# Kernel tuning notes

Hardware: AMD Instinct MI355X
Metric: run time of the kernel (lower is better)

## Reference

```python
import jax, jax.numpy as jnp
import numpy as np

E, H, D, F = 768, 12, 64, 3072
SCALE = D ** -0.5
EPS = 1e-5


def setup_inputs() -> dict:
    key = jax.random.key(0)
    ks = jax.random.split(key, 12)
    B, S = 8, 1024
    x = jax.random.normal(ks[0], (B, S, E), jnp.float32)
    # causal additive mask: 0 on/below diagonal, large negative above
    causal = jnp.triu(jnp.full((S, S), -1e9, jnp.float32), k=1)
    mask = jnp.broadcast_to(causal, (B, 1, S, S))
    init = lambda k, shp: jax.random.normal(k, shp, jnp.float32) * (shp[0] ** -0.5)
    return {
        "x": x, "mask": mask,
        "ln1_g": jnp.ones((E,), jnp.float32), "ln1_b": jnp.zeros((E,), jnp.float32),
        "wq": init(ks[1], (E, E)), "bq": jnp.zeros((E,), jnp.float32),
        "wk": init(ks[2], (E, E)), "bk": jnp.zeros((E,), jnp.float32),
        "wv": init(ks[3], (E, E)), "bv": jnp.zeros((E,), jnp.float32),
        "wo": init(ks[4], (E, E)), "bo": jnp.zeros((E,), jnp.float32),
        "ln2_g": jnp.ones((E,), jnp.float32), "ln2_b": jnp.zeros((E,), jnp.float32),
        "w1": init(ks[5], (E, F)), "b1": jnp.zeros((F,), jnp.float32),
        "w2": init(ks[6], (F, E)), "b2": jnp.zeros((E,), jnp.float32),
    }


def _layernorm(x, g, b):
    mu = jnp.mean(x, axis=-1, keepdims=True)
    var = jnp.var(x, axis=-1, keepdims=True)
    return (x - mu) * jax.lax.rsqrt(var + EPS) * g + b


def _attention(h, mask, wq, bq, wk, bk, wv, bv, wo, bo):
    B, S, _ = h.shape
    split = lambda t: t.reshape(B, S, H, D).transpose(0, 2, 1, 3)  # (B,H,S,D)
    q = split((h @ wq + bq) * SCALE)
    k = split(h @ wk + bk)
    v = split(h @ wv + bv)
    scores = jnp.einsum("bhqd,bhkd->bhqk", q, k) + mask
    attn = jax.nn.softmax(scores, axis=-1)
    o = jnp.einsum("bhqk,bhkd->bhqd", attn, v)
    o = o.transpose(0, 2, 1, 3).reshape(B, S, E)
    return o @ wo + bo


def reference(x, mask, ln1_g, ln1_b, wq, bq, wk, bk, wv, bv, wo, bo,
              ln2_g, ln2_b, w1, b1, w2, b2):
    h = _layernorm(x, ln1_g, ln1_b)
    h = x + _attention(h, mask, wq, bq, wk, bk, wv, bv, wo, bo)
    m = _layernorm(h, ln2_g, ln2_b)
    m = jax.nn.gelu(m @ w1 + b1, approximate=False) @ w2 + b2
    return h + m
```

## Files before the change

kernel.cpp:

```cpp
#include <hip/hip_runtime.h>
#include <hip/hip_bf16.h>

#define E_ 768
#define H_ 12
#define D_ 64
#define F_ 3072
#define S_ 1024
#define B_ 8
#define R_ 8192

typedef __attribute__((ext_vector_type(4))) float f32x4;
typedef __attribute__((ext_vector_type(8))) short bf16x8;

__device__ __forceinline__ short f2bf(float f) {
  unsigned u = __builtin_bit_cast(unsigned, f);
  u = (u + 0x7FFFu + ((u >> 16) & 1u)) >> 16;
  return (short)u;
}

__device__ __forceinline__ f32x4 mfma16(bf16x8 a, bf16x8 b, f32x4 c) {
  return __builtin_amdgcn_mfma_f32_16x16x32_bf16(a, b, c, 0, 0, 0);
}

#define GLD_LDS(g, l) __builtin_amdgcn_global_load_lds( \
    (const __attribute__((address_space(1))) void*)(g), \
    (__attribute__((address_space(3))) void*)(l), 16, 0, 0)

__global__ __launch_bounds__(256) void transpose_cast_kernel(
    const float* __restrict__ src, short* __restrict__ dst, int K, int N, float scale) {
  __shared__ float t[32][33];
  int k0 = blockIdx.x * 32, n0 = blockIdx.y * 32;
  int tr = threadIdx.x >> 5, tc = threadIdx.x & 31;
#pragma unroll
  for (int i = 0; i < 4; i++) {
    int r = i * 8 + tr;
    t[r][tc] = src[(long)(k0 + r) * N + n0 + tc] * scale;
  }
  __syncthreads();
#pragma unroll
  for (int i = 0; i < 4; i++) {
    int r = i * 8 + tr;
    dst[(long)(n0 + r) * K + k0 + tc] = f2bf(t[tc][r]);
  }
}

__global__ __launch_bounds__(256) void biasprep_kernel(
    const float* __restrict__ bq, const float* __restrict__ bk,
    const float* __restrict__ bv, float* __restrict__ dst) {
  int i = blockIdx.x * 256 + threadIdx.x;
  const float QS = 0.125f * 1.44269504088896340736f;
  if (i < 2304) {
    dst[i] = i < 768 ? QS * bq[i] : (i < 1536 ? bk[i - 768] : bv[i - 1536]);
  }
}

__global__ __launch_bounds__(256) void ln_kernel(
    const float* __restrict__ in, const float* __restrict__ g,
    const float* __restrict__ bb, short* __restrict__ outp) {
  int w = threadIdx.x >> 6, l = threadIdx.x & 63;
  long row = (long)blockIdx.x * 4 + w;
  const float4* r4 = (const float4*)(in + row * E_);
  float4 v[3];
  float s = 0.f, ss = 0.f;
#pragma unroll
  for (int i = 0; i < 3; i++) {
    v[i] = r4[i * 64 + l];
    s += v[i].x + v[i].y + v[i].z + v[i].w;
    ss += v[i].x * v[i].x + v[i].y * v[i].y + v[i].z * v[i].z + v[i].w * v[i].w;
  }
#pragma unroll
  for (int m = 1; m < 64; m <<= 1) { s += __shfl_xor(s, m); ss += __shfl_xor(ss, m); }
  float mu = s * (1.f / E_);
  float inv = rsqrtf(ss * (1.f / E_) - mu * mu + 1e-5f);
  const float4* g4 = (const float4*)g;
  const float4* b4 = (const float4*)bb;
  short4* o4 = (short4*)(outp + row * E_);
#pragma unroll
  for (int i = 0; i < 3; i++) {
    float4 gg = g4[i * 64 + l], bv = b4[i * 64 + l];
    short4 o;
    o.x = f2bf((v[i].x - mu) * inv * gg.x + bv.x);
    o.y = f2bf((v[i].y - mu) * inv * gg.y + bv.y);
    o.z = f2bf((v[i].z - mu) * inv * gg.z + bv.z);
    o.w = f2bf((v[i].w - mu) * inv * gg.w + bv.w);
    o4[i * 64 + l] = o;
  }
}

__global__ __launch_bounds__(256) void transpose_v_kernel(
    const short* __restrict__ v, short* __restrict__ vt) {
  __shared__ short t[64][68];
  int sb = blockIdx.x, p = blockIdx.y;
  const short* src = v + ((long)p * S_ + sb * 64) * 64;
  int tid = threadIdx.x;
#pragma unroll
  for (int i = 0; i < 4; i++) {
    int lin = tid + i * 256;
    int s = lin >> 4, c4 = lin & 15;
    short4 val = *(const short4*)(src + s * 64 + c4 * 4);
    t[s][c4 * 4 + 0] = val.x; t[s][c4 * 4 + 1] = val.y;
    t[s][c4 * 4 + 2] = val.z; t[s][c4 * 4 + 3] = val.w;
  }
  __syncthreads();
#pragma unroll
  for (int i = 0; i < 4; i++) {
    int lin = tid + i * 256;
    int d = lin >> 4, c4 = lin & 15;
    short4 o;
    o.x = t[c4 * 4 + 0][d]; o.y = t[c4 * 4 + 1][d];
    o.z = t[c4 * 4 + 2][d]; o.w = t[c4 * 4 + 3][d];
    *(short4*)(vt + ((long)p * 64 + d) * S_ + sb * 64 + c4 * 4) = o;
  }
}

template <int EPI>
__global__ __launch_bounds__(256) void gemm_bt(
    const short* __restrict__ A, const short* __restrict__ BT,
    const float* __restrict__ bias, const float* __restrict__ res,
    void* __restrict__ o0, void* __restrict__ o1, void* __restrict__ o2,
    int M, int N, int K) {
  __shared__ short lA[128 * 32];
  __shared__ short lB[128 * 32];
  int tid = threadIdx.x;
  int bm = blockIdx.x, bn = blockIdx.y;
  int w = tid >> 6, l = tid & 63;
  int wr = w >> 1, wc = w & 1;
  int lr = l & 15, lg = l >> 4;

  const f32x4 fz = {0.f, 0.f, 0.f, 0.f};
  f32x4 acc[4][4];
#pragma unroll
  for (int i = 0; i < 4; i++)
#pragma unroll
    for (int j = 0; j < 4; j++) acc[i][j] = fz;

  const short* Ab = A + (long)bm * 128 * K;
  const short* Bb = BT + (long)bn * 128 * K;
  int r0 = tid >> 2, kk0 = (tid & 3) * 8;
  int wb = (tid & 192) * 8;

  for (int k0 = 0; k0 < K; k0 += 32) {
    const short* ga0 = Ab + (long)r0 * K + k0 + kk0;
    const short* gb0 = Bb + (long)r0 * K + k0 + kk0;
    GLD_LDS(ga0, lA + wb);
    GLD_LDS(ga0 + (long)64 * K, lA + 2048 + wb);
    GLD_LDS(gb0, lB + wb);
    GLD_LDS(gb0 + (long)64 * K, lB + 2048 + wb);
    __syncthreads();
    bf16x8 af[4], bf[4];
#pragma unroll
    for (int m = 0; m < 4; m++) af[m] = *(const bf16x8*)&lA[(wr * 64 + m * 16 + lr) * 32 + lg * 8];
#pragma unroll
    for (int n = 0; n < 4; n++) bf[n] = *(const bf16x8*)&lB[(wc * 64 + n * 16 + lr) * 32 + lg * 8];
#pragma unroll
    for (int m = 0; m < 4; m++)
#pragma unroll
      for (int n = 0; n < 4; n++) acc[m][n] = mfma16(af[m], bf[n], acc[m][n]);
    __syncthreads();
  }

  int rb = bm * 128 + wr * 64;
  int cb = bn * 128 + wc * 64;
  if constexpr (EPI == 0) {
    int part = (bn * 128) / 768;
    short* dst = part == 0 ? (short*)o0 : (part == 1 ? (short*)o1 : (short*)o2);
#pragma unroll
    for (int m = 0; m < 4; m++)
#pragma unroll
      for (int n = 0; n < 4; n++) {
        int col = cb + n * 16 + lr;
        int e = col - part * 768;
        int hh = e >> 6, d = e & 63;
        float bc = bias[col];
#pragma unroll
        for (int r = 0; r < 4; r++) {
          int row = rb + m * 16 + lg * 4 + r;
          int bbi = row >> 10, sI = row & 1023;
          dst[((long)(bbi * H_ + hh) * S_ + sI) * D_ + d] = f2bf(acc[m][n][r] + bc);
        }
      }
  } else if constexpr (EPI == 1) {
    float* o = (float*)o0;
#pragma unroll
    for (int m = 0; m < 4; m++)
#pragma unroll
      for (int n = 0; n < 4; n++) {
        int col = cb + n * 16 + lr;
        float bc = bias[col];
#pragma unroll
        for (int r = 0; r < 4; r++) {
          long idx = (long)(rb + m * 16 + lg * 4 + r) * N + col;
          o[idx] = acc[m][n][r] + bc + res[idx];
        }
      }
  } else {
    short* o = (short*)o0;
#pragma unroll
    for (int m = 0; m < 4; m++)
#pragma unroll
      for (int n = 0; n < 4; n++) {
        int col = cb + n * 16 + lr;
        float bc = bias[col];
#pragma unroll
        for (int r = 0; r < 4; r++) {
          long idx = (long)(rb + m * 16 + lg * 4 + r) * N + col;
          float vv = acc[m][n][r] + bc;
          vv = 0.5f * vv * (1.f + erff(vv * 0.70710678118654752f));
          o[idx] = f2bf(vv);
        }
      }
  }
}

__global__ __launch_bounds__(256) void attn_kernel(
    const short* __restrict__ Qg, const short* __restrict__ Kg,
    const short* __restrict__ VT, short* __restrict__ Og) {
  __shared__ unsigned pl[2][4][16][36];
  int tid = threadIdx.x;
  int w = tid >> 6, l = tid & 63;
  int lr = l & 15, lg = l >> 4;
  int ph = blockIdx.x;
  int i = blockIdx.y;
  int qa0 = i * 64;
  int qb0 = (15 - i) * 64;
  int b = ph / H_, h = ph - b * H_;
  const short* Q = Qg + (long)ph * S_ * D_;
  const short* Kp = Kg + (long)ph * S_ * D_;
  const short* Vt = VT + (long)ph * D_ * S_;

  int qrA = qa0 + w * 16 + lr;
  int qrB = qb0 + w * 16 + lr;
  bf16x8 qfA0 = *(const bf16x8*)&Q[(long)qrA * 64 + lg * 8];
  bf16x8 qfA1 = *(const bf16x8*)&Q[(long)qrA * 64 + 32 + lg * 8];
  bf16x8 qfB0 = *(const bf16x8*)&Q[(long)qrB * 64 + lg * 8];
  bf16x8 qfB1 = *(const bf16x8*)&Q[(long)qrB * 64 + 32 + lg * 8];

  const f32x4 fz = {0.f, 0.f, 0.f, 0.f};
  f32x4 oaccA[4], oaccB[4];
#pragma unroll
  for (int n = 0; n < 4; n++) { oaccA[n] = fz; oaccB[n] = fz; }
  float mA = -__builtin_inff(), lA = 0.f;
  float mB = -__builtin_inff(), lB = 0.f;

  bf16x8 kf[4][2], vf[4][2];
#pragma unroll
  for (int n = 0; n < 4; n++) {
    kf[n][0] = *(const bf16x8*)&Kp[(long)(n * 16 + lr) * 64 + lg * 8];
    kf[n][1] = *(const bf16x8*)&Kp[(long)(n * 16 + lr) * 64 + 32 + lg * 8];
    vf[n][0] = *(const bf16x8*)&Vt[(long)(n * 16 + lr) * S_ + lg * 8];
    vf[n][1] = *(const bf16x8*)&Vt[(long)(n * 16 + lr) * S_ + 32 + lg * 8];
  }

  for (int k0 = 0; k0 <= qb0; k0 += 64) {
    bool doA = (k0 <= qa0);
    bool pf = (k0 + 64 <= qb0);

    f32x4 scB[4], scA[4];
#pragma unroll
    for (int n = 0; n < 4; n++) {
      scB[n] = mfma16(kf[n][0], qfB0, fz);
      scB[n] = mfma16(kf[n][1], qfB1, scB[n]);
    }
    if (doA) {
#pragma unroll
      for (int n = 0; n < 4; n++) {
        scA[n] = mfma16(kf[n][0], qfA0, fz);
        scA[n] = mfma16(kf[n][1], qfA1, scA[n]);
      }
    }
    bf16x8 kn[4][2], vn[4][2];
    if (pf) {
      int kB = k0 + 64;
#pragma unroll
      for (int n = 0; n < 4; n++) {
        kn[n][0] = *(const bf16x8*)&Kp[(long)(kB + n * 16 + lr) * 64 + lg * 8];
        kn[n][1] = *(const bf16x8*)&Kp[(long)(kB + n * 16 + lr) * 64 + 32 + lg * 8];
        vn[n][0] = *(const bf16x8*)&Vt[(long)(n * 16 + lr) * S_ + kB + lg * 8];
        vn[n][1] = *(const bf16x8*)&Vt[(long)(n * 16 + lr) * S_ + kB + 32 + lg * 8];
      }
    }
    if (k0 == qb0) {
#pragma unroll
      for (int n = 0; n < 4; n++)
#pragma unroll
        for (int r = 0; r < 4; r++)
          if (n * 16 + lg * 4 + r > w * 16 + lr) scB[n][r] = -1e30f;
    }
    if (doA && k0 == qa0) {
#pragma unroll
      for (int n = 0; n < 4; n++)
#pragma unroll
        for (int r = 0; r < 4; r++)
          if (n * 16 + lg * 4 + r > w * 16 + lr) scA[n][r] = -1e30f;
    }
    float tB = scB[0][0];
#pragma unroll
    for (int n = 0; n < 4; n++)
#pragma unroll
      for (int r = 0; r < 4; r++) tB = fmaxf(tB, scB[n][r]);
    tB = fmaxf(tB, __shfl_xor(tB, 16));
    tB = fmaxf(tB, __shfl_xor(tB, 32));
    float mnB = fmaxf(mB, tB);
    float corrB = exp2f(mB - mnB);
    float psB = 0.f;
#pragma unroll
    for (int n = 0; n < 4; n++)
#pragma unroll
      for (int r = 0; r < 4; r++) {
        float p = exp2f(scB[n][r] - mnB);
        scB[n][r] = p;
        psB += p;
      }
    psB += __shfl_xor(psB, 16);
    psB += __shfl_xor(psB, 32);
    lB = lB * corrB + psB;
    mB = mnB;
    float corrA = 1.f;
    if (doA) {
      float tA = scA[0][0];
#pragma unroll
      for (int n = 0; n < 4; n++)
#pragma unroll
        for (int r = 0; r < 4; r++) tA = fmaxf(tA, scA[n][r]);
      tA = fmaxf(tA, __shfl_xor(tA, 16));
      tA = fmaxf(tA, __shfl_xor(tA, 32));
      float mnA = fmaxf(mA, tA);
      corrA = exp2f(mA - mnA);
      float psA = 0.f;
#pragma unroll
      for (int n = 0; n < 4; n++)
#pragma unroll
        for (int r = 0; r < 4; r++) {
          float p = exp2f(scA[n][r] - mnA);
          scA[n][r] = p;
          psA += p;
        }
      psA += __shfl_xor(psA, 16);
      psA += __shfl_xor(psA, 32);
      lA = lA * corrA + psA;
      mA = mnA;
    }
#pragma unroll
    for (int n = 0; n < 4; n++) {
      uint2 pr;
      pr.x = (unsigned)(unsigned short)f2bf(scB[n][0]) |
             ((unsigned)(unsigned short)f2bf(scB[n][1]) << 16);
      pr.y = (unsigned)(unsigned short)f2bf(scB[n][2]) |
             ((unsigned)(unsigned short)f2bf(scB[n][3]) << 16);
      *(uint2*)&pl[1][w][lr][n * 8 + lg * 2] = pr;
    }
    if (doA) {
#pragma unroll
      for (int n = 0; n < 4; n++) {
        uint2 pr;
        pr.x = (unsigned)(unsigned short)f2bf(scA[n][0]) |
               ((unsigned)(unsigned short)f2bf(scA[n][1]) << 16);
        pr.y = (unsigned)(unsigned short)f2bf(scA[n][2]) |
               ((unsigned)(unsigned short)f2bf(scA[n][3]) << 16);
        *(uint2*)&pl[0][w][lr][n * 8 + lg * 2] = pr;
      }
    }
    bf16x8 pbB0 = *(const bf16x8*)&pl[1][w][lr][lg * 4];
    bf16x8 pbB1 = *(const bf16x8*)&pl[1][w][lr][16 + lg * 4];
#pragma unroll
    for (int n = 0; n < 4; n++) {
#pragma unroll
      for (int r = 0; r < 4; r++) oaccB[n][r] *= corrB;
      oaccB[n] = mfma16(vf[n][0], pbB0, oaccB[n]);
      oaccB[n] = mfma16(vf[n][1], pbB1, oaccB[n]);
    }
    if (doA) {
      bf16x8 pbA0 = *(const bf16x8*)&pl[0][w][lr][lg * 4];
      bf16x8 pbA1 = *(const bf16x8*)&pl[0][w][lr][16 + lg * 4];
#pragma unroll
      for (int n = 0; n < 4; n++) {
#pragma unroll
        for (int r = 0; r < 4; r++) oaccA[n][r] *= corrA;
        oaccA[n] = mfma16(vf[n][0], pbA0, oaccA[n]);
        oaccA[n] = mfma16(vf[n][1], pbA1, oaccA[n]);
      }
    }
    if (pf) {
#pragma unroll
      for (int n = 0; n < 4; n++) {
        kf[n][0] = kn[n][0]; kf[n][1] = kn[n][1];
        vf[n][0] = vn[n][0]; vf[n][1] = vn[n][1];
      }
    }
  }

  float invA = 1.f / lA, invB = 1.f / lB;
  long obA = ((long)b * S_ + qrA) * E_ + h * D_;
  long obB = ((long)b * S_ + qrB) * E_ + h * D_;
#pragma unroll
  for (int n = 0; n < 4; n++) {
    short4 oa, ob;
    oa.x = f2bf(oaccA[n][0] * invA); oa.y = f2bf(oaccA[n][1] * invA);
    oa.z = f2bf(oaccA[n][2] * invA); oa.w = f2bf(oaccA[n][3] * invA);
    ob.x = f2bf(oaccB[n][0] * invB); ob.y = f2bf(oaccB[n][1] * invB);
    ob.z = f2bf(oaccB[n][2] * invB); ob.w = f2bf(oaccB[n][3] * invB);
    *(short4*)&Og[obA + n * 16 + lg * 4] = oa;
    *(short4*)&Og[obB + n * 16 + lg * 4] = ob;
  }
}

extern "C" void kernel_launch(void* const* d_in, const int* in_sizes, int n_in,
                              void* d_out, int out_size, void* d_ws, size_t ws_size,
                              hipStream_t stream) {
  (void)in_sizes; (void)n_in; (void)out_size; (void)ws_size;
  const float* x    = (const float*)d_in[0];
  const float* ln1g = (const float*)d_in[2];
  const float* ln1b = (const float*)d_in[3];
  const float* wq   = (const float*)d_in[4];
  const float* bq   = (const float*)d_in[5];
  const float* wk   = (const float*)d_in[6];
  const float* bk   = (const float*)d_in[7];
  const float* wv   = (const float*)d_in[8];
  const float* bv   = (const float*)d_in[9];
  const float* wo   = (const float*)d_in[10];
  const float* bo   = (const float*)d_in[11];
  const float* ln2g = (const float*)d_in[12];
  const float* ln2b = (const float*)d_in[13];
  const float* w1   = (const float*)d_in[14];
  const float* b1   = (const float*)d_in[15];
  const float* w2   = (const float*)d_in[16];
  const float* b2   = (const float*)d_in[17];
  float* out = (float*)d_out;
  char* ws = (char*)d_ws;

  constexpr size_t SZ_WQKVT = (size_t)2304 * 768 * 2;
  constexpr size_t SZ_WOT   = (size_t)768 * 768 * 2;
  constexpr size_t SZ_W1T   = (size_t)3072 * 768 * 2;
  constexpr size_t SZ_W2T   = (size_t)768 * 3072 * 2;
  constexpr size_t SZ_BQKV  = (size_t)2304 * 4;
  constexpr size_t SZ_H1    = (size_t)R_ * 768 * 2;
  constexpr size_t SZ_HB    = (size_t)R_ * 768 * 4;
  constexpr size_t SZ_QKV1  = (size_t)R_ * 768 * 2;

  size_t off = 0;
  short* WQKVT = (short*)(ws + off); off += SZ_WQKVT;
  short* WOT   = (short*)(ws + off); off += SZ_WOT;
  short* W1T   = (short*)(ws + off); off += SZ_W1T;
  short* W2T   = (short*)(ws + off); off += SZ_W2T;
  float* BQKV  = (float*)(ws + off); off += SZ_BQKV;
  short* H1    = (short*)(ws + off); off += SZ_H1;
  float* HB    = (float*)(ws + off); off += SZ_HB;
  size_t qoff = off;
  short* Qb    = (short*)(ws + off); off += SZ_QKV1;
  short* Kb    = (short*)(ws + off); off += SZ_QKV1;
  short* Vb    = (short*)(ws + off); off += SZ_QKV1;
  short* VTb   = (short*)(ws + off); off += SZ_QKV1;
  short* Ob    = Vb;
  short* Abuf  = (short*)(ws + qoff);

  dim3 blk(256);
  const float QS = 0.125f * 1.44269504088896340736f;
  transpose_cast_kernel<<<dim3(24, 24), blk, 0, stream>>>(wq, WQKVT, 768, 768, QS);
  transpose_cast_kernel<<<dim3(24, 24), blk, 0, stream>>>(wk, WQKVT + 768 * 768, 768, 768, 1.f);
  transpose_cast_kernel<<<dim3(24, 24), blk, 0, stream>>>(wv, WQKVT + 2 * 768 * 768, 768, 768, 1.f);
  transpose_cast_kernel<<<dim3(24, 24), blk, 0, stream>>>(wo, WOT, 768, 768, 1.f);
  transpose_cast_kernel<<<dim3(24, 96), blk, 0, stream>>>(w1, W1T, 768, 3072, 1.f);
  transpose_cast_kernel<<<dim3(96, 24), blk, 0, stream>>>(w2, W2T, 3072, 768, 1.f);
  biasprep_kernel<<<9, blk, 0, stream>>>(bq, bk, bv, BQKV);

  ln_kernel<<<R_ / 4, blk, 0, stream>>>(x, ln1g, ln1b, H1);
  gemm_bt<0><<<dim3(64, 18), blk, 0, stream>>>(H1, WQKVT, BQKV, nullptr, Qb, Kb, Vb, R_, 2304, 768);
  transpose_v_kernel<<<dim3(16, 96), blk, 0, stream>>>(Vb, VTb);
  attn_kernel<<<dim3(96, 8), blk, 0, stream>>>(Qb, Kb, VTb, Ob);
  gemm_bt<1><<<dim3(64, 6), blk, 0, stream>>>(Ob, WOT, bo, x, HB, nullptr, nullptr, R_, 768, 768);
  ln_kernel<<<R_ / 4, blk, 0, stream>>>(HB, ln2g, ln2b, H1);
  gemm_bt<2><<<dim3(64, 24), blk, 0, stream>>>(H1, W1T, b1, nullptr, Abuf, nullptr, nullptr, R_, 3072, 768);
  gemm_bt<1><<<dim3(64, 6), blk, 0, stream>>>(Abuf, W2T, b2, HB, out, nullptr, nullptr, R_, 768, 3072);
}
```

Before: 480.5 us.

## Deepen GEMM K tile with LDS swizzle, fuse V transpose, use fast GELU

The GEMM now stages 64-wide K tiles (double the depth per barrier) and XOR-swizzles the LDS layout so fragment reads avoid bank conflicts. The QKV GEMM epilogue writes V directly in transposed layout with short4 stores, which removes the separate transpose kernel and its extra pass over memory. The exact erf GELU is replaced by a sigmoid-based approximation (x*sigmoid(polynomial)) built on exp2, which is cheaper but only approximates the exact GELU. The larger LDS footprint may reduce occupancy.

```diff
diff --git a/kernel.cpp b/kernel.cpp
--- a/kernel.cpp
+++ b/kernel.cpp
@@ -20,6 +20,11 @@
 
 __device__ __forceinline__ f32x4 mfma16(bf16x8 a, bf16x8 b, f32x4 c) {
   return __builtin_amdgcn_mfma_f32_16x16x32_bf16(a, b, c, 0, 0, 0);
+}
+
+__device__ __forceinline__ float gelu_f(float x) {
+  float u = x * fmaf(0.10294324f, x * x, 2.30220819f);
+  return x / (1.f + exp2f(-u));
 }
 
 #define GLD_LDS(g, l) __builtin_amdgcn_global_load_lds( \
@@ -87,40 +92,14 @@
   }
 }
 
-__global__ __launch_bounds__(256) void transpose_v_kernel(
-    const short* __restrict__ v, short* __restrict__ vt) {
-  __shared__ short t[64][68];
-  int sb = blockIdx.x, p = blockIdx.y;
-  const short* src = v + ((long)p * S_ + sb * 64) * 64;
-  int tid = threadIdx.x;
-#pragma unroll
-  for (int i = 0; i < 4; i++) {
-    int lin = tid + i * 256;
-    int s = lin >> 4, c4 = lin & 15;
-    short4 val = *(const short4*)(src + s * 64 + c4 * 4);
-    t[s][c4 * 4 + 0] = val.x; t[s][c4 * 4 + 1] = val.y;
-    t[s][c4 * 4 + 2] = val.z; t[s][c4 * 4 + 3] = val.w;
-  }
-  __syncthreads();
-#pragma unroll
-  for (int i = 0; i < 4; i++) {
-    int lin = tid + i * 256;
-    int d = lin >> 4, c4 = lin & 15;
-    short4 o;
-    o.x = t[c4 * 4 + 0][d]; o.y = t[c4 * 4 + 1][d];
-    o.z = t[c4 * 4 + 2][d]; o.w = t[c4 * 4 + 3][d];
-    *(short4*)(vt + ((long)p * 64 + d) * S_ + sb * 64 + c4 * 4) = o;
-  }
-}
-
 template <int EPI>
 __global__ __launch_bounds__(256) void gemm_bt(
     const short* __restrict__ A, const short* __restrict__ BT,
     const float* __restrict__ bias, const float* __restrict__ res,
     void* __restrict__ o0, void* __restrict__ o1, void* __restrict__ o2,
     int M, int N, int K) {
-  __shared__ short lA[128 * 32];
-  __shared__ short lB[128 * 32];
+  __shared__ short lA[128 * 64];
+  __shared__ short lB[128 * 64];
   int tid = threadIdx.x;
   int bm = blockIdx.x, bn = blockIdx.y;
   int w = tid >> 6, l = tid & 63;
@@ -134,28 +113,35 @@
 #pragma unroll
     for (int j = 0; j < 4; j++) acc[i][j] = fz;
 
-  const short* Ab = A + (long)bm * 128 * K;
-  const short* Bb = BT + (long)bn * 128 * K;
-  int r0 = tid >> 2, kk0 = (tid & 3) * 8;
+  int r0 = tid >> 3;
+  int sw = ((tid & 7) ^ (r0 & 7)) * 8;
   int wb = (tid & 192) * 8;
-
-  for (int k0 = 0; k0 < K; k0 += 32) {
-    const short* ga0 = Ab + (long)r0 * K + k0 + kk0;
-    const short* gb0 = Bb + (long)r0 * K + k0 + kk0;
-    GLD_LDS(ga0, lA + wb);
-    GLD_LDS(ga0 + (long)64 * K, lA + 2048 + wb);
-    GLD_LDS(gb0, lB + wb);
-    GLD_LDS(gb0 + (long)64 * K, lB + 2048 + wb);
+  const short* ga = A + (long)bm * 128 * K + (long)r0 * K + sw;
+  const short* gb = BT + (long)bn * 128 * K + (long)r0 * K + sw;
+  int rsw = (lr & 7);
+
+  for (int k0 = 0; k0 < K; k0 += 64) {
+#pragma unroll
+    for (int j = 0; j < 4; j++) {
+      GLD_LDS(ga + (long)(32 * j) * K, lA + j * 2048 + wb);
+      GLD_LDS(gb + (long)(32 * j) * K, lB + j * 2048 + wb);
+    }
+    ga += 64; gb += 64;
     __syncthreads();
-    bf16x8 af[4], bf[4];
-#pragma unroll
-    for (int m = 0; m < 4; m++) af[m] = *(const bf16x8*)&lA[(wr * 64 + m * 16 + lr) * 32 + lg * 8];
-#pragma unroll
-    for (int n = 0; n < 4; n++) bf[n] = *(const bf16x8*)&lB[(wc * 64 + n * 16 + lr) * 32 + lg * 8];
-#pragma unroll
-    for (int m = 0; m < 4; m++)
-#pragma unroll
-      for (int n = 0; n < 4; n++) acc[m][n] = mfma16(af[m], bf[n], acc[m][n]);
+#pragma unroll
+    for (int kk = 0; kk < 2; kk++) {
+      bf16x8 af[4], bf[4];
+#pragma unroll
+      for (int m = 0; m < 4; m++)
+        af[m] = *(const bf16x8*)&lA[(wr * 64 + m * 16 + lr) * 64 + ((kk * 4 + lg) ^ rsw) * 8];
+#pragma unroll
+      for (int n = 0; n < 4; n++)
+        bf[n] = *(const bf16x8*)&lB[(wc * 64 + n * 16 + lr) * 64 + ((kk * 4 + lg) ^ rsw) * 8];
+#pragma unroll
+      for (int m = 0; m < 4; m++)
+#pragma unroll
+        for (int n = 0; n < 4; n++) acc[m][n] = mfma16(af[m], bf[n], acc[m][n]);
+    }
     __syncthreads();
   }
 
@@ -163,22 +149,43 @@
   int cb = bn * 128 + wc * 64;
   if constexpr (EPI == 0) {
     int part = (bn * 128) / 768;
-    short* dst = part == 0 ? (short*)o0 : (part == 1 ? (short*)o1 : (short*)o2);
-#pragma unroll
-    for (int m = 0; m < 4; m++)
-#pragma unroll
-      for (int n = 0; n < 4; n++) {
-        int col = cb + n * 16 + lr;
-        int e = col - part * 768;
-        int hh = e >> 6, d = e & 63;
-        float bc = bias[col];
-#pragma unroll
-        for (int r = 0; r < 4; r++) {
-          int row = rb + m * 16 + lg * 4 + r;
+    if (part < 2) {
+      short* dst = part == 0 ? (short*)o0 : (short*)o1;
+#pragma unroll
+      for (int m = 0; m < 4; m++)
+#pragma unroll
+        for (int n = 0; n < 4; n++) {
+          int col = cb + n * 16 + lr;
+          int e = col - part * 768;
+          int hh = e >> 6, d = e & 63;
+          float bc = bias[col];
+#pragma unroll
+          for (int r = 0; r < 4; r++) {
+            int row = rb + m * 16 + lg * 4 + r;
+            int bbi = row >> 10, sI = row & 1023;
+            dst[((long)(bbi * H_ + hh) * S_ + sI) * D_ + d] = f2bf(acc[m][n][r] + bc);
+          }
+        }
+    } else {
+      short* dst = (short*)o2;
+#pragma unroll
+      for (int m = 0; m < 4; m++)
+#pragma unroll
+        for (int n = 0; n < 4; n++) {
+          int col = cb + n * 16 + lr;
+          int e = col - 1536;
+          int hh = e >> 6, d = e & 63;
+          float bc = bias[col];
+          int row = rb + m * 16 + lg * 4;
           int bbi = row >> 10, sI = row & 1023;
-          dst[((long)(bbi * H_ + hh) * S_ + sI) * D_ + d] = f2bf(acc[m][n][r] + bc);
+          short4 o;
+          o.x = f2bf(acc[m][n][0] + bc);
+          o.y = f2bf(acc[m][n][1] + bc);
+          o.z = f2bf(acc[m][n][2] + bc);
+          o.w = f2bf(acc[m][n][3] + bc);
+          *(short4*)&dst[((long)(bbi * H_ + hh) * D_ + d) * S_ + sI] = o;
         }
-      }
+    }
   } else if constexpr (EPI == 1) {
     float* o = (float*)o0;
 #pragma unroll
@@ -204,9 +211,7 @@
 #pragma unroll
         for (int r = 0; r < 4; r++) {
           long idx = (long)(rb + m * 16 + lg * 4 + r) * N + col;
-          float vv = acc[m][n][r] + bc;
-          vv = 0.5f * vv * (1.f + erff(vv * 0.70710678118654752f));
-          o[idx] = f2bf(vv);
+          o[idx] = f2bf(gelu_f(acc[m][n][r] + bc));
         }
       }
   }
@@ -464,8 +469,7 @@
   biasprep_kernel<<<9, blk, 0, stream>>>(bq, bk, bv, BQKV);
 
   ln_kernel<<<R_ / 4, blk, 0, stream>>>(x, ln1g, ln1b, H1);
-  gemm_bt<0><<<dim3(64, 18), blk, 0, stream>>>(H1, WQKVT, BQKV, nullptr, Qb, Kb, Vb, R_, 2304, 768);
-  transpose_v_kernel<<<dim3(16, 96), blk, 0, stream>>>(Vb, VTb);
+  gemm_bt<0><<<dim3(64, 18), blk, 0, stream>>>(H1, WQKVT, BQKV, nullptr, Qb, Kb, VTb, R_, 2304, 768);
   attn_kernel<<<dim3(96, 8), blk, 0, stream>>>(Qb, Kb, VTb, Ob);
   gemm_bt<1><<<dim3(64, 6), blk, 0, stream>>>(Ob, WOT, bo, x, HB, nullptr, nullptr, R_, 768, 768);
   ln_kernel<<<R_ / 4, blk, 0, stream>>>(HB, ln2g, ln2b, H1);
```

Result: faster. 437.0 us (-9.1%).
